# Kernel tuning notes

Measured on AMD Instinct MI355X. Metric: run time of the kernel, lower is better.

The kernel has to match this reference:

```python
import jax, jax.numpy as jnp
import numpy as np

B, S, F, DV, H, DH, L = 32, 600, 9, 1024, 16, 64, 2


def setup_inputs() -> dict:
    key = jax.random.key(0)
    ks = jax.random.split(key, 24)
    w = lambda k, shape, s=0.05: jax.random.normal(k, shape, dtype=jnp.float32) * s
    return {
        "x": w(ks[0], (B, S, F), 1.0),
        "enc_in_W": w(ks[1], (F, DV)), "enc_in_b": w(ks[2], (DV,)),
        "Wq": w(ks[3], (L, H, DV, DH)), "bq": w(ks[4], (L, H, DH)),
        "Wk": w(ks[5], (L, H, DV, DH)), "bk": w(ks[6], (L, H, DH)),
        "Wv": w(ks[7], (L, H, DV, DH)), "bv": w(ks[8], (L, H, DH)),
        "Wo": w(ks[9], (L, DV, DV)), "bo": w(ks[10], (L, DV)),
        "W1": w(ks[11], (L, DV, DV)), "b1": w(ks[12], (L, DV)),
        "W2": w(ks[13], (L, DV, DV)), "b2": w(ks[14], (L, DV)),
        "ln1_w": jnp.ones((L, DV)), "ln1_b": jnp.zeros((L, DV)),
        "ln2_w": jnp.ones((L, DV)), "ln2_b": jnp.zeros((L, DV)),
        "out_W": w(ks[15], (DV, F)), "out_b": w(ks[16], (F,)),
    }


def _layernorm(v, g, b):
    mu = v.mean(-1, keepdims=True)
    var = v.var(-1, keepdims=True)  # biased, matches torch LayerNorm
    return (v - mu) / jnp.sqrt(var + 1e-5) * g + b


def reference(x, enc_in_W, enc_in_b, Wq, bq, Wk, bk, Wv, bv, Wo, bo,
              W1, b1, W2, b2, ln1_w, ln1_b, ln2_w, ln2_b, out_W, out_b):
    # enc_input_fc; pe skipped (code checks pe_mode == 'stardard', never true)
    h = x @ enc_in_W + enc_in_b  # [B,S,DV]
    scale = 1.0 / jnp.sqrt(jnp.float32(DH))
    for l in range(L):
        q = jnp.einsum('bsd,hdk->bhsk', h, Wq[l]) + bq[l][None, :, None, :]
        k = jnp.einsum('bsd,hdk->bhsk', h, Wk[l]) + bk[l][None, :, None, :]
        v = jnp.einsum('bsd,hdk->bhsk', h, Wv[l]) + bv[l][None, :, None, :]
        attn = jax.nn.softmax(jnp.einsum('bhsk,bhtk->bhst', q, k) * scale, axis=-1)
        ctx = jnp.einsum('bhst,bhtk->bhsk', attn, v)  # [B,H,S,DH]
        # torch: stack(heads, dim=-1) -> [B,S,DH,H], then flatten(start_dim=2)
        a = ctx.transpose(0, 2, 3, 1).reshape(B, S, DH * H)
        attn_out = a @ Wo[l] + bo[l]
        x1 = _layernorm(h + attn_out, ln1_w[l], ln1_b[l])
        ff = jax.nn.elu(x1 @ W2[l] + b2[l]) @ W1[l] + b1[l]  # fc1(elu(fc2(x1)))
        h = _layernorm(x1 + ff, ln2_w[l], ln2_b[l])
    out = h @ out_W + out_b  # [B,S,F]; in_seq_len == out_seq_len -> no out_seq_fc
    return out
```

## Files before the change

### kernel.cpp

```cpp
#include <hip/hip_runtime.h>

typedef unsigned short u16;
typedef unsigned int u32;
typedef __attribute__((ext_vector_type(8))) short shortx8;
typedef __attribute__((ext_vector_type(4))) float floatx4;
typedef __attribute__((ext_vector_type(4))) u32 uintx4;
typedef __attribute__((ext_vector_type(2))) u32 uintx2;

#define AS1 __attribute__((address_space(1)))
#define AS3 __attribute__((address_space(3)))

__device__ __forceinline__ float bf2f(u16 u) {
  return __builtin_bit_cast(float, ((u32)u) << 16);
}
__device__ __forceinline__ u16 f2bf(float f) {
  u32 i = __builtin_bit_cast(u32, f);
  u32 r = (i + 0x7fffu + ((i >> 16) & 1u)) >> 16;
  return (u16)r;
}

__launch_bounds__(256)
__global__ void pack_qkv_t(const float* __restrict__ W, u16* __restrict__ dst) {
  __shared__ u16 T[64][72];
  const int kt = blockIdx.x, y = blockIdx.y;
  const int l = y >> 4, h = y & 15;
  const int t = threadIdx.x;
  const int rr = t >> 2, cq = (t & 3) * 16;
  const float* src = W + ((size_t)y * 1024 + kt * 64 + rr) * 64 + cq;
#pragma unroll
  for (int e4 = 0; e4 < 4; ++e4) {
    float4 f = *(const float4*)(src + e4 * 4);
    T[cq + e4 * 4 + 0][rr] = f2bf(f.x);
    T[cq + e4 * 4 + 1][rr] = f2bf(f.y);
    T[cq + e4 * 4 + 2][rr] = f2bf(f.z);
    T[cq + e4 * 4 + 3][rr] = f2bf(f.w);
  }
  __syncthreads();
  const int dd = t >> 2, kq = (t & 3) * 16;
  u16* drow = dst + (size_t)l * 3145728 + ((size_t)h * 64 + dd) * 1024 + kt * 64 + kq;
  *(uintx4*)(drow) = *(const uintx4*)&T[dd][kq];
  *(uintx4*)(drow + 8) = *(const uintx4*)&T[dd][kq + 8];
}

__launch_bounds__(256)
__global__ void pack_sq_t(const float* __restrict__ W, u16* __restrict__ dst) {
  __shared__ u16 T[64][72];
  const int ct = blockIdx.x & 15, rt = blockIdx.x >> 4, l = blockIdx.y;
  const int t = threadIdx.x;
  const int rr = t >> 2, cq = (t & 3) * 16;
  const float* src = W + (size_t)l * 1048576 + (size_t)(rt * 64 + rr) * 1024 + ct * 64 + cq;
#pragma unroll
  for (int e4 = 0; e4 < 4; ++e4) {
    float4 f = *(const float4*)(src + e4 * 4);
    T[cq + e4 * 4 + 0][rr] = f2bf(f.x);
    T[cq + e4 * 4 + 1][rr] = f2bf(f.y);
    T[cq + e4 * 4 + 2][rr] = f2bf(f.z);
    T[cq + e4 * 4 + 3][rr] = f2bf(f.w);
  }
  __syncthreads();
  const int cc = t >> 2, rq = (t & 3) * 16;
  u16* drow = dst + (size_t)l * 1048576 + (size_t)(ct * 64 + cc) * 1024 + rt * 64 + rq;
  *(uintx4*)(drow) = *(const uintx4*)&T[cc][rq];
  *(uintx4*)(drow + 8) = *(const uintx4*)&T[cc][rq + 8];
}

__launch_bounds__(256)
__global__ void pack_bias(const float* __restrict__ bq, const float* __restrict__ bk,
                          const float* __restrict__ bv, float* __restrict__ bias) {
  const int i = blockIdx.x * 256 + threadIdx.x;
  const int l = i / 3072, n = i % 3072;
  const int which = n >> 10, nn = n & 1023;
  const float* s = (which == 0) ? bq : (which == 1) ? bk : bv;
  bias[i] = s[l * 1024 + nn];
}

__launch_bounds__(256)
__global__ void enc_kernel(const float* __restrict__ x, const float* __restrict__ W,
                           const float* __restrict__ bias, u16* __restrict__ h) {
  const size_t i = (size_t)blockIdx.x * 256 + threadIdx.x;
  const int m = (int)(i >> 10), n = (int)(i & 1023);
  const float* xr = x + (size_t)m * 9;
  float acc = bias[n];
#pragma unroll
  for (int f = 0; f < 9; ++f) acc += xr[f] * W[f * 1024 + n];
  h[i] = f2bf(acc);
}

template <int EPI>
__launch_bounds__(256)
__global__ void gemm_bt(const u16* __restrict__ A, int lda,
                        const u16* __restrict__ Bt,
                        const float* __restrict__ bias,
                        const u16* __restrict__ R, int ldr,
                        u16* __restrict__ C, int ldc) {
  constexpr int K = 1024;
  __shared__ u16 As[128 * 64];
  __shared__ u16 Bs[128 * 64];
  const int tid = threadIdx.x;
  const int lane = tid & 63;
  const int w = tid >> 6;
  const int wr = w >> 1, wc = w & 1;
  const int m0 = blockIdx.y * 128, n0 = blockIdx.x * 128;

  floatx4 acc[4][4];
#pragma unroll
  for (int i = 0; i < 4; ++i)
#pragma unroll
    for (int j = 0; j < 4; ++j) acc[i][j] = (floatx4){0.f, 0.f, 0.f, 0.f};

  const u16* Ab = A + (size_t)m0 * lda;
  const u16* Bb = Bt + (size_t)n0 * K;

  for (int k0 = 0; k0 < K; k0 += 64) {
#pragma unroll
    for (int p = 0; p < 4; ++p) {
      const int o = p * 4096 + tid * 16;
      const int row = o >> 7;
      const int ke = (o & 127) >> 1;
      __builtin_amdgcn_global_load_lds((const AS1 void*)(Ab + (size_t)row * lda + (k0 + ke)),
                                       (AS3 void*)((char*)As + o), 16, 0, 0);
      __builtin_amdgcn_global_load_lds((const AS1 void*)(Bb + (size_t)row * K + (k0 + ke)),
                                       (AS3 void*)((char*)Bs + o), 16, 0, 0);
    }
    __syncthreads();
#pragma unroll
    for (int ks = 0; ks < 2; ++ks) {
      shortx8 af[4], bfr[4];
#pragma unroll
      for (int i = 0; i < 4; ++i) {
        const int ar = wr * 64 + i * 16 + (lane & 15);
        af[i] = *(const shortx8*)&As[ar * 64 + ks * 32 + (lane >> 4) * 8];
        const int br = wc * 64 + i * 16 + (lane & 15);
        bfr[i] = *(const shortx8*)&Bs[br * 64 + ks * 32 + (lane >> 4) * 8];
      }
#pragma unroll
      for (int i = 0; i < 4; ++i)
#pragma unroll
        for (int j = 0; j < 4; ++j)
          acc[i][j] = __builtin_amdgcn_mfma_f32_16x16x32_bf16(af[i], bfr[j], acc[i][j], 0, 0, 0);
    }
    __syncthreads();
  }

  const int lr = (lane >> 4) * 4, lc = lane & 15;
#pragma unroll
  for (int i = 0; i < 4; ++i) {
#pragma unroll
    for (int j = 0; j < 4; ++j) {
      const int col = n0 + wc * 64 + j * 16 + lc;
      const float bv = bias[col];
#pragma unroll
      for (int r = 0; r < 4; ++r) {
        const int row = m0 + wr * 64 + i * 16 + lr + r;
        float v = acc[i][j][r] + bv;
        if (EPI == 1) v += bf2f(R[(size_t)row * ldr + col]);
        if (EPI == 2) v = v > 0.f ? v : expm1f(v);
        C[(size_t)row * ldc + col] = f2bf(v);
      }
    }
  }
}

__launch_bounds__(512)
__global__ void gemm_bt_wide(const u16* __restrict__ A, int lda,
                             const u16* __restrict__ Bt,
                             const float* __restrict__ bias,
                             u16* __restrict__ C, int ldc) {
  constexpr int K = 1024;
  __shared__ u16 As[128 * 64];
  __shared__ u16 Bs[256 * 64];
  const int tid = threadIdx.x;
  const int lane = tid & 63;
  const int w = tid >> 6;
  const int wr = w >> 2, wc = w & 3;
  const int m0 = blockIdx.y * 128, n0 = blockIdx.x * 256;

  floatx4 acc[4][4];
#pragma unroll
  for (int i = 0; i < 4; ++i)
#pragma unroll
    for (int j = 0; j < 4; ++j) acc[i][j] = (floatx4){0.f, 0.f, 0.f, 0.f};

  const u16* Ab = A + (size_t)m0 * lda;
  const u16* Bb = Bt + (size_t)n0 * K;

  for (int k0 = 0; k0 < K; k0 += 64) {
#pragma unroll
    for (int p = 0; p < 2; ++p) {
      const int o = p * 8192 + tid * 16;
      const int row = o >> 7;
      const int ke = (o & 127) >> 1;
      __builtin_amdgcn_global_load_lds((const AS1 void*)(Ab + (size_t)row * lda + (k0 + ke)),
                                       (AS3 void*)((char*)As + o), 16, 0, 0);
    }
#pragma unroll
    for (int p = 0; p < 4; ++p) {
      const int o = p * 8192 + tid * 16;
      const int row = o >> 7;
      const int ke = (o & 127) >> 1;
      __builtin_amdgcn_global_load_lds((const AS1 void*)(Bb + (size_t)row * K + (k0 + ke)),
                                       (AS3 void*)((char*)Bs + o), 16, 0, 0);
    }
    __syncthreads();
#pragma unroll
    for (int ks = 0; ks < 2; ++ks) {
      shortx8 af[4], bfr[4];
#pragma unroll
      for (int i = 0; i < 4; ++i) {
        const int ar = wr * 64 + i * 16 + (lane & 15);
        af[i] = *(const shortx8*)&As[ar * 64 + ks * 32 + (lane >> 4) * 8];
        const int br = wc * 64 + i * 16 + (lane & 15);
        bfr[i] = *(const shortx8*)&Bs[br * 64 + ks * 32 + (lane >> 4) * 8];
      }
#pragma unroll
      for (int i = 0; i < 4; ++i)
#pragma unroll
        for (int j = 0; j < 4; ++j)
          acc[i][j] = __builtin_amdgcn_mfma_f32_16x16x32_bf16(af[i], bfr[j], acc[i][j], 0, 0, 0);
    }
    __syncthreads();
  }

  const int lr = (lane >> 4) * 4, lc = lane & 15;
#pragma unroll
  for (int i = 0; i < 4; ++i) {
#pragma unroll
    for (int j = 0; j < 4; ++j) {
      const int col = n0 + wc * 64 + j * 16 + lc;
      const float bv = bias[col];
#pragma unroll
      for (int r = 0; r < 4; ++r) {
        const int row = m0 + wr * 64 + i * 16 + lr + r;
        C[(size_t)row * ldc + col] = f2bf(acc[i][j][r] + bv);
      }
    }
  }
}

__launch_bounds__(256)
__global__ void attn_mfma(const u16* __restrict__ qkv, u16* __restrict__ aout) {
  const int qt = blockIdx.x, bh = blockIdx.y;
  const int b = bh >> 4, h = bh & 15;
  const int tid = threadIdx.x, lane = tid & 63, w = tid >> 6;
  const int g = lane >> 4, lq = lane & 15;

  __shared__ u16 K_ld[128 * 72];
  __shared__ u16 Vt[64 * 136];
  __shared__ u16 P_ld[4][16 * 136];

  const size_t bbase = (size_t)b * 600 * 3072;
  const int q0 = qt * 64 + w * 16;

  shortx8 aq[2];
  {
    const int s = q0 + lq;
    if (s < 600) {
      const u16* qp = qkv + bbase + (size_t)s * 3072 + h * 64 + g * 8;
      aq[0] = *(const shortx8*)qp;
      aq[1] = *(const shortx8*)(qp + 32);
    } else {
      aq[0] = (shortx8){0, 0, 0, 0, 0, 0, 0, 0};
      aq[1] = (shortx8){0, 0, 0, 0, 0, 0, 0, 0};
    }
  }

  floatx4 Oa[4];
#pragma unroll
  for (int db = 0; db < 4; ++db) Oa[db] = (floatx4){0.f, 0.f, 0.f, 0.f};
  float m[4], l[4];
#pragma unroll
  for (int r = 0; r < 4; ++r) { m[r] = -1e30f; l[r] = 0.f; }

  for (int ch = 0; ch < 5; ++ch) {
    const int t0 = ch * 128;
    __syncthreads();
    {
      const int tloc = tid >> 1, dhalf = (tid & 1) * 32;
      const int tg = t0 + tloc;
      if (tg < 600) {
        const u16* kp = qkv + bbase + (size_t)tg * 3072 + 1024 + h * 64 + dhalf;
        const u16* vp = kp + 1024;
#pragma unroll
        for (int c = 0; c < 4; ++c)
          *(uintx4*)&K_ld[tloc * 72 + dhalf + c * 8] = *(const uintx4*)(kp + c * 8);
#pragma unroll
        for (int c = 0; c < 4; ++c) {
          shortx8 vv = *(const shortx8*)(vp + c * 8);
#pragma unroll
          for (int e = 0; e < 8; ++e)
            Vt[(dhalf + c * 8 + e) * 136 + tloc] = (u16)vv[e];
        }
      } else {
        const uintx4 z4 = (uintx4){0, 0, 0, 0};
#pragma unroll
        for (int c = 0; c < 4; ++c)
          *(uintx4*)&K_ld[tloc * 72 + dhalf + c * 8] = z4;
#pragma unroll
        for (int c = 0; c < 4; ++c)
#pragma unroll
          for (int e = 0; e < 8; ++e)
            Vt[(dhalf + c * 8 + e) * 136 + tloc] = 0;
      }
    }
    __syncthreads();

    floatx4 S[8];
#pragma unroll
    for (int jb = 0; jb < 8; ++jb) {
      S[jb] = (floatx4){0.f, 0.f, 0.f, 0.f};
#pragma unroll
      for (int ks = 0; ks < 2; ++ks) {
        shortx8 bk = *(const shortx8*)&K_ld[(jb * 16 + lq) * 72 + ks * 32 + g * 8];
        S[jb] = __builtin_amdgcn_mfma_f32_16x16x32_bf16(aq[ks], bk, S[jb], 0, 0, 0);
      }
    }
#pragma unroll
    for (int jb = 0; jb < 8; ++jb) {
      const int tg = t0 + jb * 16 + lq;
      const bool ok = tg < 600;
#pragma unroll
      for (int r = 0; r < 4; ++r) S[jb][r] = ok ? S[jb][r] * 0.125f : -1e30f;
    }

    float scale[4];
#pragma unroll
    for (int r = 0; r < 4; ++r) {
      float v = S[0][r];
#pragma unroll
      for (int jb = 1; jb < 8; ++jb) v = fmaxf(v, S[jb][r]);
      v = fmaxf(v, __shfl_xor(v, 1));
      v = fmaxf(v, __shfl_xor(v, 2));
      v = fmaxf(v, __shfl_xor(v, 4));
      v = fmaxf(v, __shfl_xor(v, 8));
      const float mn = fmaxf(m[r], v);
      scale[r] = __expf(m[r] - mn);
      m[r] = mn;
      l[r] *= scale[r];
    }
#pragma unroll
    for (int db = 0; db < 4; ++db)
#pragma unroll
      for (int r = 0; r < 4; ++r) Oa[db][r] *= scale[r];

    float sums[4] = {0.f, 0.f, 0.f, 0.f};
#pragma unroll
    for (int jb = 0; jb < 8; ++jb)
#pragma unroll
      for (int r = 0; r < 4; ++r) {
        const float p = __expf(S[jb][r] - m[r]);
        sums[r] += p;
        P_ld[w][(g * 4 + r) * 136 + jb * 16 + lq] = f2bf(p);
      }
#pragma unroll
    for (int r = 0; r < 4; ++r) {
      float v = sums[r];
      v += __shfl_xor(v, 1);
      v += __shfl_xor(v, 2);
      v += __shfl_xor(v, 4);
      v += __shfl_xor(v, 8);
      l[r] += v;
    }

#pragma unroll
    for (int ks = 0; ks < 4; ++ks) {
      shortx8 ap = *(const shortx8*)&P_ld[w][lq * 136 + ks * 32 + g * 8];
#pragma unroll
      for (int db = 0; db < 4; ++db) {
        shortx8 bv = *(const shortx8*)&Vt[(db * 16 + lq) * 136 + ks * 32 + g * 8];
        Oa[db] = __builtin_amdgcn_mfma_f32_16x16x32_bf16(ap, bv, Oa[db], 0, 0, 0);
      }
    }
  }

#pragma unroll
  for (int r = 0; r < 4; ++r) {
    const int sg = q0 + g * 4 + r;
    if (sg < 600) {
      const float inv = 1.f / l[r];
      u16* orow = aout + ((size_t)(b * 600 + sg)) * 1024 + h;
#pragma unroll
      for (int db = 0; db < 4; ++db)
        orow[(size_t)(db * 16 + lq) * 16] = f2bf(Oa[db][r] * inv);
    }
  }
}

__launch_bounds__(256)
__global__ void ln_kernel(const u16* __restrict__ y, int ldy,
                          const float* __restrict__ g, const float* __restrict__ be,
                          u16* __restrict__ o, int ldo) {
  const int row = blockIdx.x, tid = threadIdx.x;
  const int lane = tid & 63, wv = tid >> 6;
  const u16* yr = y + (size_t)row * ldy;
  const int c = tid * 4;
  const uintx2 yv = *(const uintx2*)&yr[c];
  float v0 = bf2f((u16)(yv[0] & 0xffffu)), v1 = bf2f((u16)(yv[0] >> 16));
  float v2 = bf2f((u16)(yv[1] & 0xffffu)), v3 = bf2f((u16)(yv[1] >> 16));
  float s = v0 + v1 + v2 + v3;
  float q = v0 * v0 + v1 * v1 + v2 * v2 + v3 * v3;
#pragma unroll
  for (int m = 32; m; m >>= 1) {
    s += __shfl_xor(s, m);
    q += __shfl_xor(q, m);
  }
  __shared__ float red[2][4];
  if (lane == 0) {
    red[0][wv] = s;
    red[1][wv] = q;
  }
  __syncthreads();
  s = red[0][0] + red[0][1] + red[0][2] + red[0][3];
  q = red[1][0] + red[1][1] + red[1][2] + red[1][3];
  const float mu = s * (1.f / 1024.f);
  const float var = q * (1.f / 1024.f) - mu * mu;
  const float rstd = rsqrtf(var + 1e-5f);
  const float4 gv = *(const float4*)&g[c];
  const float4 bev = *(const float4*)&be[c];
  const float o0 = (v0 - mu) * rstd * gv.x + bev.x;
  const float o1 = (v1 - mu) * rstd * gv.y + bev.y;
  const float o2 = (v2 - mu) * rstd * gv.z + bev.z;
  const float o3 = (v3 - mu) * rstd * gv.w + bev.w;
  uintx2 ov;
  ov[0] = (u32)f2bf(o0) | ((u32)f2bf(o1) << 16);
  ov[1] = (u32)f2bf(o2) | ((u32)f2bf(o3) << 16);
  *(uintx2*)&o[(size_t)row * ldo + c] = ov;
}

__launch_bounds__(256)
__global__ void out_kernel(const u16* __restrict__ h, const float* __restrict__ W,
                           const float* __restrict__ bias, float* __restrict__ out) {
  const int m = blockIdx.x * 4 + (threadIdx.x >> 6);
  const int lane = threadIdx.x & 63;
  float acc[9];
#pragma unroll
  for (int f = 0; f < 9; ++f) acc[f] = 0.f;
  const u16* hr = h + (size_t)m * 1024;
#pragma unroll 4
  for (int j = 0; j < 16; ++j) {
    const int k = lane + j * 64;
    const float hv = bf2f(hr[k]);
    const float* wr = W + (size_t)k * 9;
#pragma unroll
    for (int f = 0; f < 9; ++f) acc[f] += hv * wr[f];
  }
#pragma unroll
  for (int f = 0; f < 9; ++f)
#pragma unroll
    for (int mm = 32; mm; mm >>= 1) acc[f] += __shfl_xor(acc[f], mm);
  if (lane < 9) out[(size_t)m * 9 + lane] = acc[lane] + bias[lane];
}

extern "C" void kernel_launch(void* const* d_in, const int* in_sizes, int n_in,
                              void* d_out, int out_size, void* d_ws, size_t ws_size,
                              hipStream_t stream) {
  (void)in_sizes; (void)n_in; (void)out_size; (void)ws_size;
  const float* x     = (const float*)d_in[0];
  const float* encW  = (const float*)d_in[1];
  const float* encB  = (const float*)d_in[2];
  const float* Wq    = (const float*)d_in[3];
  const float* bq    = (const float*)d_in[4];
  const float* Wk    = (const float*)d_in[5];
  const float* bk    = (const float*)d_in[6];
  const float* Wv    = (const float*)d_in[7];
  const float* bv    = (const float*)d_in[8];
  const float* Wo    = (const float*)d_in[9];
  const float* bo    = (const float*)d_in[10];
  const float* W1    = (const float*)d_in[11];
  const float* b1    = (const float*)d_in[12];
  const float* W2    = (const float*)d_in[13];
  const float* b2    = (const float*)d_in[14];
  const float* ln1w  = (const float*)d_in[15];
  const float* ln1b  = (const float*)d_in[16];
  const float* ln2w  = (const float*)d_in[17];
  const float* ln2b  = (const float*)d_in[18];
  const float* outW  = (const float*)d_in[19];
  const float* outB  = (const float*)d_in[20];
  float* out = (float*)d_out;

  char* ws = (char*)d_ws;
  size_t off = 0;
  auto alloc = [&](size_t bytes) -> void* {
    void* p = ws + off;
    off += (bytes + 255) & ~(size_t)255;
    return p;
  };
  u16* h    = (u16*)alloc(19660800ull * 2);
  u16* qkv  = (u16*)alloc(58982400ull * 2);
  u16* abuf = (u16*)alloc(19660800ull * 2);
  u16* Bqkv = (u16*)alloc(6291456ull * 2);
  u16* Bwo  = (u16*)alloc(2097152ull * 2);
  u16* Bw1  = (u16*)alloc(2097152ull * 2);
  u16* Bw2  = (u16*)alloc(2097152ull * 2);
  float* bqkv = (float*)alloc(6144ull * 4);
  u16* ybuf = qkv;
  u16* x1   = qkv + 1024;
  u16* mid  = qkv + 2048;
  u16* y2   = abuf;

  pack_qkv_t<<<dim3(16, 32), 256, 0, stream>>>(Wq, Bqkv);
  pack_qkv_t<<<dim3(16, 32), 256, 0, stream>>>(Wk, Bqkv + 1048576);
  pack_qkv_t<<<dim3(16, 32), 256, 0, stream>>>(Wv, Bqkv + 2097152);
  pack_sq_t<<<dim3(256, 2), 256, 0, stream>>>(Wo, Bwo);
  pack_sq_t<<<dim3(256, 2), 256, 0, stream>>>(W1, Bw1);
  pack_sq_t<<<dim3(256, 2), 256, 0, stream>>>(W2, Bw2);
  pack_bias<<<24, 256, 0, stream>>>(bq, bk, bv, bqkv);
  enc_kernel<<<76800, 256, 0, stream>>>(x, encW, encB, h);

  for (int l = 0; l < 2; ++l) {
    gemm_bt_wide<<<dim3(12, 150), 512, 0, stream>>>(
        h, 1024, Bqkv + (size_t)l * 3145728, bqkv + l * 3072, qkv, 3072);
    attn_mfma<<<dim3(10, 512), 256, 0, stream>>>(qkv, abuf);
    gemm_bt<1><<<dim3(8, 150), 256, 0, stream>>>(
        abuf, 1024, Bwo + (size_t)l * 1048576, bo + l * 1024, h, 1024, ybuf, 3072);
    ln_kernel<<<19200, 256, 0, stream>>>(ybuf, 3072, ln1w + l * 1024, ln1b + l * 1024, x1, 3072);
    gemm_bt<2><<<dim3(8, 150), 256, 0, stream>>>(
        x1, 3072, Bw2 + (size_t)l * 1048576, b2 + l * 1024, nullptr, 0, mid, 3072);
    gemm_bt<1><<<dim3(8, 150), 256, 0, stream>>>(
        mid, 3072, Bw1 + (size_t)l * 1048576, b1 + l * 1024, x1, 3072, y2, 1024);
    ln_kernel<<<19200, 256, 0, stream>>>(y2, 1024, ln2w + l * 1024, ln2b + l * 1024, h, 1024);
  }
  out_kernel<<<4800, 256, 0, stream>>>(h, outW, outB, out);
}
```

Measured before the change: 1.327 ms.

## Double query rows per attention block and store head-contiguous context with permuted Wo

New measurement: 1.288 ms. -3.0%, faster.

```diff
diff --git a/kernel.cpp b/kernel.cpp
--- a/kernel.cpp
+++ b/kernel.cpp
@@ -62,6 +62,35 @@
   u16* drow = dst + (size_t)l * 1048576 + (size_t)(ct * 64 + cc) * 1024 + rt * 64 + rq;
   *(uintx4*)(drow) = *(const uintx4*)&T[cc][rq];
   *(uintx4*)(drow + 8) = *(const uintx4*)&T[cc][rq + 8];
+}
+
+__launch_bounds__(256)
+__global__ void pack_wo_t(const float* __restrict__ W, u16* __restrict__ dst) {
+  __shared__ u16 T[64][72];
+  const int rt = blockIdx.x >> 4, nt = blockIdx.x & 15, l = blockIdx.y;
+  const int t = threadIdx.x;
+  const int rr = t >> 2, cq = (t & 3) * 16;
+  const float* src = W + (size_t)l * 1048576 + (size_t)(rt * 64 + rr) * 1024 + nt * 64 + cq;
+#pragma unroll
+  for (int e4 = 0; e4 < 4; ++e4) {
+    float4 f = *(const float4*)(src + e4 * 4);
+    T[cq + e4 * 4 + 0][rr] = f2bf(f.x);
+    T[cq + e4 * 4 + 1][rr] = f2bf(f.y);
+    T[cq + e4 * 4 + 2][rr] = f2bf(f.z);
+    T[cq + e4 * 4 + 3][rr] = f2bf(f.w);
+  }
+  __syncthreads();
+  const int hh = t & 15;
+#pragma unroll
+  for (int pass = 0; pass < 4; ++pass) {
+    const int nl = pass * 16 + (t >> 4);
+    uintx2 pk;
+    u16 v0 = T[nl][0 * 16 + hh], v1 = T[nl][1 * 16 + hh];
+    u16 v2 = T[nl][2 * 16 + hh], v3 = T[nl][3 * 16 + hh];
+    pk[0] = (u32)v0 | ((u32)v1 << 16);
+    pk[1] = (u32)v2 | ((u32)v3 << 16);
+    *(uintx2*)&dst[(size_t)l * 1048576 + (size_t)(nt * 64 + nl) * 1024 + hh * 64 + rt * 4] = pk;
+  }
 }
 
 __launch_bounds__(256)
@@ -249,27 +278,31 @@
   __shared__ u16 P_ld[4][16 * 136];
 
   const size_t bbase = (size_t)b * 600 * 3072;
-  const int q0 = qt * 64 + w * 16;
-
-  shortx8 aq[2];
-  {
-    const int s = q0 + lq;
+  const int q0 = qt * 128 + w * 32;
+
+  shortx8 aq[2][2];
+#pragma unroll
+  for (int sub = 0; sub < 2; ++sub) {
+    const int s = q0 + sub * 16 + lq;
     if (s < 600) {
       const u16* qp = qkv + bbase + (size_t)s * 3072 + h * 64 + g * 8;
-      aq[0] = *(const shortx8*)qp;
-      aq[1] = *(const shortx8*)(qp + 32);
+      aq[sub][0] = *(const shortx8*)qp;
+      aq[sub][1] = *(const shortx8*)(qp + 32);
     } else {
-      aq[0] = (shortx8){0, 0, 0, 0, 0, 0, 0, 0};
-      aq[1] = (shortx8){0, 0, 0, 0, 0, 0, 0, 0};
-    }
-  }
-
-  floatx4 Oa[4];
-#pragma unroll
-  for (int db = 0; db < 4; ++db) Oa[db] = (floatx4){0.f, 0.f, 0.f, 0.f};
-  float m[4], l[4];
-#pragma unroll
-  for (int r = 0; r < 4; ++r) { m[r] = -1e30f; l[r] = 0.f; }
+      aq[sub][0] = (shortx8){0, 0, 0, 0, 0, 0, 0, 0};
+      aq[sub][1] = (shortx8){0, 0, 0, 0, 0, 0, 0, 0};
+    }
+  }
+
+  floatx4 Oa[2][4];
+  float m[2][4], l[2][4];
+#pragma unroll
+  for (int sub = 0; sub < 2; ++sub) {
+#pragma unroll
+    for (int db = 0; db < 4; ++db) Oa[sub][db] = (floatx4){0.f, 0.f, 0.f, 0.f};
+#pragma unroll
+    for (int r = 0; r < 4; ++r) { m[sub][r] = -1e30f; l[sub][r] = 0.f; }
+  }
 
   for (int ch = 0; ch < 5; ++ch) {
     const int t0 = ch * 128;
@@ -304,83 +337,89 @@
     }
     __syncthreads();
 
-    floatx4 S[8];
-#pragma unroll
-    for (int jb = 0; jb < 8; ++jb) {
-      S[jb] = (floatx4){0.f, 0.f, 0.f, 0.f};
-#pragma unroll
-      for (int ks = 0; ks < 2; ++ks) {
-        shortx8 bk = *(const shortx8*)&K_ld[(jb * 16 + lq) * 72 + ks * 32 + g * 8];
-        S[jb] = __builtin_amdgcn_mfma_f32_16x16x32_bf16(aq[ks], bk, S[jb], 0, 0, 0);
-      }
-    }
-#pragma unroll
-    for (int jb = 0; jb < 8; ++jb) {
-      const int tg = t0 + jb * 16 + lq;
-      const bool ok = tg < 600;
-#pragma unroll
-      for (int r = 0; r < 4; ++r) S[jb][r] = ok ? S[jb][r] * 0.125f : -1e30f;
-    }
-
-    float scale[4];
+#pragma unroll
+    for (int sub = 0; sub < 2; ++sub) {
+      floatx4 S[8];
+#pragma unroll
+      for (int jb = 0; jb < 8; ++jb) {
+        S[jb] = (floatx4){0.f, 0.f, 0.f, 0.f};
+#pragma unroll
+        for (int ks = 0; ks < 2; ++ks) {
+          shortx8 bk = *(const shortx8*)&K_ld[(jb * 16 + lq) * 72 + ks * 32 + g * 8];
+          S[jb] = __builtin_amdgcn_mfma_f32_16x16x32_bf16(aq[sub][ks], bk, S[jb], 0, 0, 0);
+        }
+      }
+#pragma unroll
+      for (int jb = 0; jb < 8; ++jb) {
+        const int tg = t0 + jb * 16 + lq;
+        const bool ok = tg < 600;
+#pragma unroll
+        for (int r = 0; r < 4; ++r) S[jb][r] = ok ? S[jb][r] * 0.125f : -1e30f;
+      }
+
+      float scale[4];
+#pragma unroll
+      for (int r = 0; r < 4; ++r) {
+        float v = S[0][r];
+#pragma unroll
+        for (int jb = 1; jb < 8; ++jb) v = fmaxf(v, S[jb][r]);
+        v = fmaxf(v, __shfl_xor(v, 1));
+        v = fmaxf(v, __shfl_xor(v, 2));
+        v = fmaxf(v, __shfl_xor(v, 4));
+        v = fmaxf(v, __shfl_xor(v, 8));
+        const float mn = fmaxf(m[sub][r], v);
+        scale[r] = __expf(m[sub][r] - mn);
+        m[sub][r] = mn;
+        l[sub][r] *= scale[r];
+      }
+#pragma unroll
+      for (int db = 0; db < 4; ++db)
+#pragma unroll
+        for (int r = 0; r < 4; ++r) Oa[sub][db][r] *= scale[r];
+
+      float sums[4] = {0.f, 0.f, 0.f, 0.f};
+#pragma unroll
+      for (int jb = 0; jb < 8; ++jb)
+#pragma unroll
+        for (int r = 0; r < 4; ++r) {
+          const float p = __expf(S[jb][r] - m[sub][r]);
+          sums[r] += p;
+          P_ld[w][(g * 4 + r) * 136 + jb * 16 + lq] = f2bf(p);
+        }
+#pragma unroll
+      for (int r = 0; r < 4; ++r) {
+        float v = sums[r];
+        v += __shfl_xor(v, 1);
+        v += __shfl_xor(v, 2);
+        v += __shfl_xor(v, 4);
+        v += __shfl_xor(v, 8);
+        l[sub][r] += v;
+      }
+
+#pragma unroll
+      for (int ks = 0; ks < 4; ++ks) {
+        shortx8 ap = *(const shortx8*)&P_ld[w][lq * 136 + ks * 32 + g * 8];
+#pragma unroll
+        for (int db = 0; db < 4; ++db) {
+          shortx8 bv = *(const shortx8*)&Vt[(db * 16 + lq) * 136 + ks * 32 + g * 8];
+          Oa[sub][db] = __builtin_amdgcn_mfma_f32_16x16x32_bf16(ap, bv, Oa[sub][db], 0, 0, 0);
+        }
+      }
+    }
+  }
+
+#pragma unroll
+  for (int sub = 0; sub < 2; ++sub) {
 #pragma unroll
     for (int r = 0; r < 4; ++r) {
-      float v = S[0][r];
-#pragma unroll
-      for (int jb = 1; jb < 8; ++jb) v = fmaxf(v, S[jb][r]);
-      v = fmaxf(v, __shfl_xor(v, 1));
-      v = fmaxf(v, __shfl_xor(v, 2));
-      v = fmaxf(v, __shfl_xor(v, 4));
-      v = fmaxf(v, __shfl_xor(v, 8));
-      const float mn = fmaxf(m[r], v);
-      scale[r] = __expf(m[r] - mn);
-      m[r] = mn;
-      l[r] *= scale[r];
-    }
-#pragma unroll
-    for (int db = 0; db < 4; ++db)
-#pragma unroll
-      for (int r = 0; r < 4; ++r) Oa[db][r] *= scale[r];
-
-    float sums[4] = {0.f, 0.f, 0.f, 0.f};
-#pragma unroll
-    for (int jb = 0; jb < 8; ++jb)
-#pragma unroll
-      for (int r = 0; r < 4; ++r) {
-        const float p = __expf(S[jb][r] - m[r]);
-        sums[r] += p;
-        P_ld[w][(g * 4 + r) * 136 + jb * 16 + lq] = f2bf(p);
-      }
-#pragma unroll
-    for (int r = 0; r < 4; ++r) {
-      float v = sums[r];
-      v += __shfl_xor(v, 1);
-      v += __shfl_xor(v, 2);
-      v += __shfl_xor(v, 4);
-      v += __shfl_xor(v, 8);
-      l[r] += v;
-    }
-
-#pragma unroll
-    for (int ks = 0; ks < 4; ++ks) {
-      shortx8 ap = *(const shortx8*)&P_ld[w][lq * 136 + ks * 32 + g * 8];
-#pragma unroll
-      for (int db = 0; db < 4; ++db) {
-        shortx8 bv = *(const shortx8*)&Vt[(db * 16 + lq) * 136 + ks * 32 + g * 8];
-        Oa[db] = __builtin_amdgcn_mfma_f32_16x16x32_bf16(ap, bv, Oa[db], 0, 0, 0);
-      }
-    }
-  }
-
-#pragma unroll
-  for (int r = 0; r < 4; ++r) {
-    const int sg = q0 + g * 4 + r;
-    if (sg < 600) {
-      const float inv = 1.f / l[r];
-      u16* orow = aout + ((size_t)(b * 600 + sg)) * 1024 + h;
-#pragma unroll
-      for (int db = 0; db < 4; ++db)
-        orow[(size_t)(db * 16 + lq) * 16] = f2bf(Oa[db][r] * inv);
+      const int sg = q0 + sub * 16 + g * 4 + r;
+      if (sg < 600) {
+        const float inv = 1.f / l[sub][r];
+        u16* orow = aout + ((size_t)(b * 600 + sg)) * 1024 + h * 64;
+#pragma unroll
+        for (int db = 0; db < 4; ++db)
+          orow[db * 16 + lq] = f2bf(Oa[sub][db][r] * inv);
+      }
     }
   }
 }
@@ -500,7 +539,7 @@
   pack_qkv_t<<<dim3(16, 32), 256, 0, stream>>>(Wq, Bqkv);
   pack_qkv_t<<<dim3(16, 32), 256, 0, stream>>>(Wk, Bqkv + 1048576);
   pack_qkv_t<<<dim3(16, 32), 256, 0, stream>>>(Wv, Bqkv + 2097152);
-  pack_sq_t<<<dim3(256, 2), 256, 0, stream>>>(Wo, Bwo);
+  pack_wo_t<<<dim3(256, 2), 256, 0, stream>>>(Wo, Bwo);
   pack_sq_t<<<dim3(256, 2), 256, 0, stream>>>(W1, Bw1);
   pack_sq_t<<<dim3(256, 2), 256, 0, stream>>>(W2, Bw2);
   pack_bias<<<24, 256, 0, stream>>>(bq, bk, bv, bqkv);
@@ -509,7 +548,7 @@
   for (int l = 0; l < 2; ++l) {
     gemm_bt_wide<<<dim3(12, 150), 512, 0, stream>>>(
         h, 1024, Bqkv + (size_t)l * 3145728, bqkv + l * 3072, qkv, 3072);
-    attn_mfma<<<dim3(10, 512), 256, 0, stream>>>(qkv, abuf);
+    attn_mfma<<<dim3(5, 512), 256, 0, stream>>>(qkv, abuf);
     gemm_bt<1><<<dim3(8, 150), 256, 0, stream>>>(
         abuf, 1024, Bwo + (size_t)l * 1048576, bo + l * 1024, h, 1024, ybuf, 3072);
     ln_kernel<<<19200, 256, 0, stream>>>(ybuf, 3072, ln1w + l * 1024, ln1b + l * 1024, x1, 3072);
```
